# Optimization experiments

Hardware: AMD Instinct MI355X
Metric: run time of the kernel (lower is better)

Reference implementation:

```python
import jax, jax.numpy as jnp
import numpy as np

MAT_MODE = ((0, 1), (0, 2), (1, 2))
VEC_MODE = (2, 1, 0)
DENSITY_SHIFT = -10.0
DISTANCE_SCALE = 25.0


def grid_sample_2d(img, coords):
    # img: [C, H, W]; coords: [N, 2] in [-1, 1], (x indexes W, y indexes H);
    # bilinear, align_corners=True (matches F.grid_sample in the source).
    C, H, W = img.shape
    x = (coords[:, 0] + 1.0) * 0.5 * (W - 1)
    y = (coords[:, 1] + 1.0) * 0.5 * (H - 1)
    x0 = jnp.floor(x)
    y0 = jnp.floor(y)
    wx = x - x0
    wy = y - y0
    x0i = jnp.clip(x0.astype(jnp.int32), 0, W - 1)
    x1i = jnp.clip(x0i + 1, 0, W - 1)
    y0i = jnp.clip(y0.astype(jnp.int32), 0, H - 1)
    y1i = jnp.clip(y0i + 1, 0, H - 1)
    v00 = img[:, y0i, x0i]
    v01 = img[:, y0i, x1i]
    v10 = img[:, y1i, x0i]
    v11 = img[:, y1i, x1i]
    return (v00 * (1 - wx) * (1 - wy) + v01 * wx * (1 - wy)
            + v10 * (1 - wx) * wy + v11 * wx * wy)  # [C, N]


def line_sample_1d(line, t):
    # line: [C, L]; t: [N] in [-1, 1]. Equivalent to the source's grid_sample on a
    # [1, C, L, 1] tensor with coords (0, t): the width dim (size 1) collapses.
    C, L = line.shape
    y = (t + 1.0) * 0.5 * (L - 1)
    y0 = jnp.floor(y)
    wy = y - y0
    y0i = jnp.clip(y0.astype(jnp.int32), 0, L - 1)
    y1i = jnp.clip(y0i + 1, 0, L - 1)
    return line[:, y0i] * (1 - wy) + line[:, y1i] * wy  # [C, N]


def tensorf_features(planes, lines, xyz):
    # planes: [3, C, H, W]; lines: [3, C, L]; xyz: [N, 3] normalized coords.
    # fusion_two='concat' then fusion_one='multiply' == per-plane multiply, concat.
    feats = []
    for i in range(3):
        a, b = MAT_MODE[i]
        pc = jnp.stack([xyz[:, a], xyz[:, b]], axis=-1)  # [N, 2]
        pf = grid_sample_2d(planes[i], pc)               # [C, N]
        lf = line_sample_1d(lines[i], xyz[:, VEC_MODE[i]])  # [C, N]
        feats.append(pf * lf)
    return jnp.concatenate(feats, axis=0)  # [3C, N]


def raw2alpha(sigma, dist):
    # sigma, dist: [Nr, Ns]
    alpha = 1.0 - jnp.exp(-sigma * dist)
    T = jnp.cumprod(jnp.concatenate(
        [jnp.ones((alpha.shape[0], 1), alpha.dtype), 1.0 - alpha + 1e-10], axis=-1), axis=-1)
    weights = alpha * T[:, :-1]
    return alpha, weights, T[:, -1:]


def setup_inputs() -> dict:
    key = jax.random.key(0)
    ks = jax.random.split(key, 10)
    Nr, Ns, G = 4096, 256, 300
    aabb = jnp.array([[-1.5, -1.5, -1.5], [1.5, 1.5, 1.5]], jnp.float32)
    xyz_sampled = jax.random.uniform(ks[0], (Nr, Ns, 3), jnp.float32,
                                     minval=-1.5, maxval=1.5)
    vd = jax.random.normal(ks[1], (Nr, 3), jnp.float32)
    viewdirs = vd / jnp.linalg.norm(vd, axis=-1, keepdims=True)
    near, far = 2.0, 6.0
    t = jnp.linspace(0.0, 1.0, Ns, dtype=jnp.float32)
    z_vals = near * (1.0 - t) + far * t
    z_vals = jnp.broadcast_to(z_vals, (Nr, Ns)) + \
        jax.random.uniform(ks[2], (Nr, Ns), jnp.float32) * ((far - near) / Ns)
    z_vals = jnp.sort(z_vals, axis=-1)
    s = 0.1  # init_scale
    return {
        'xyz_sampled': xyz_sampled,
        'viewdirs': viewdirs,
        'z_vals': z_vals,
        'density_planes': s * jax.random.normal(ks[3], (3, 8, G, G), jnp.float32),
        'density_lines': s * jax.random.normal(ks[4], (3, 8, G), jnp.float32),
        'app_planes': s * jax.random.normal(ks[5], (3, 24, G, G), jnp.float32),
        'app_lines': s * jax.random.normal(ks[6], (3, 24, G), jnp.float32),
        'density_basis_w': jnp.ones((1, 24), jnp.float32),  # source inits to 1/density_dim
        'app_basis_w': s * jax.random.normal(ks[7], (3, 72), jnp.float32),
        'aabb': aabb,
    }


def reference(xyz_sampled, viewdirs, z_vals, density_planes, density_lines,
              app_planes, app_lines, density_basis_w, app_basis_w, aabb):
    Nr, Ns, _ = xyz_sampled.shape
    # normalize_coord: map aabb -> [-1, 1]
    inv_size = 2.0 / (aabb[1] - aabb[0])
    xyz = ((xyz_sampled - aabb[0]) * inv_size - 1.0).reshape(-1, 3)  # [N, 3]

    dfeat = tensorf_features(density_planes, density_lines, xyz)      # [24, N]
    sigma_feat = (density_basis_w @ dfeat).reshape(Nr, Ns)            # basis_mat
    sigma = jax.nn.softplus(sigma_feat + DENSITY_SHIFT)               # fea2denseAct

    # ray-marching distances
    dists = z_vals[:, 1:] - z_vals[:, :-1]
    dists = jnp.concatenate([dists, dists[:, -1:]], axis=-1)
    alpha, weights, bg_T = raw2alpha(sigma, dists * DISTANCE_SCALE)

    # appearance branch: RGBRender is identity on the 3-dim basis output
    afeat = tensorf_features(app_planes, app_lines, xyz)              # [72, N]
    rgb = (app_basis_w @ afeat).T.reshape(Nr, Ns, 3)

    rgb_map = jnp.sum(weights[..., None] * rgb, axis=1)               # [Nr, 3]
    return rgb_map
```

## Files before the change

### kernel.cpp

```cpp
#include <hip/hip_runtime.h>
#include <math.h>

#define G  300
#define NS 256
#define NR 4096
#define CT 32

typedef _Float16 half16_t;
typedef _Float16 h8 __attribute__((ext_vector_type(8)));

__global__ __launch_bounds__(256) void prep_all(
    const float* __restrict__ dp, const float* __restrict__ ap,
    const float* __restrict__ dl, const float* __restrict__ al,
    half16_t* __restrict__ outp, half16_t* __restrict__ outl)
{
  int t = blockIdx.x * blockDim.x + threadIdx.x;
  if (t < 3 * G * G) {
    int x  = t % G;
    int yi = t / G;
    int y  = yi % G;
    int i  = yi / G;
    const float* dpp = dp + ((size_t)(i * 8) * G + y) * G + x;
    const float* app = ap + ((size_t)(i * 24) * G + y) * G + x;
    h8 v[4];
#pragma unroll
    for (int c = 0; c < 8; ++c) v[c >> 3][c & 7] = (half16_t)dpp[(size_t)c * G * G];
#pragma unroll
    for (int c = 0; c < 24; ++c) {
      int cc = c + 8;
      v[cc >> 3][cc & 7] = (half16_t)app[(size_t)c * G * G];
    }
    h8* o = (h8*)(outp + (size_t)t * CT);
#pragma unroll
    for (int m = 0; m < 4; ++m) o[m] = v[m];
  } else {
    int u = t - 3 * G * G;
    if (u < 3 * G) {
      int p = u % G;
      int i = u / G;
      h8 v[4];
#pragma unroll
      for (int c = 0; c < 8; ++c) v[c >> 3][c & 7] = (half16_t)dl[(i * 8 + c) * G + p];
#pragma unroll
      for (int c = 0; c < 24; ++c) {
        int cc = c + 8;
        v[cc >> 3][cc & 7] = (half16_t)al[(i * 24 + c) * G + p];
      }
      h8* o = (h8*)(outl + (size_t)u * CT);
#pragma unroll
      for (int m = 0; m < 4; ++m) o[m] = v[m];
    }
  }
}

__global__ __launch_bounds__(256) void tensorf_fused(
    const float* __restrict__ xyz, const float* __restrict__ zv,
    const half16_t* __restrict__ planes, const half16_t* __restrict__ lns,
    const float* __restrict__ dbw, const float* __restrict__ abw,
    const float* __restrict__ aabb, float* __restrict__ out)
{
  __shared__ float4 srgb[2][NS];
  __shared__ float  sW[3][128];
  __shared__ float  sTot[2];
  __shared__ float4 sSum[2][2];

  const int tid = threadIdx.x;
  for (int idx = tid; idx < 3 * 128; idx += 256) {
    int j = idx >> 7, c = idx & 127;
    float v = 0.f;
    if (c < 72) v = abw[j * 72 + c];
    else if (j == 0 && c < 96) v = dbw[c - 72];
    sW[j][c] = v;
  }
  __syncthreads();

  const int wv   = tid >> 6;
  const int lane = tid & 63;
  const int rl   = wv >> 1;
  const int hf   = wv & 1;
  const int ray  = (blockIdx.x << 1) + rl;
  const int q    = lane >> 2;
  const int r    = lane & 3;

  const float a0x = aabb[0], a0y = aabb[1], a0z = aabb[2];
  const float ivx = 2.f / (aabb[3] - aabb[0]);
  const float ivy = 2.f / (aabb[4] - aabb[1]);
  const float ivz = 2.f / (aabb[5] - aabb[2]);

  const int MA[3] = {0, 0, 1};
  const int MB[3] = {1, 2, 2};
  const int MV[3] = {2, 1, 0};

  const int ro = r * 8;

  for (int it = 0; it < 8; ++it) {
    int s = (hf << 7) + (it << 4) + q;
    const float* xp = xyz + ((size_t)ray * NS + s) * 3;
    float g[3];
    g[0] = (xp[0] - a0x) * ivx - 1.f;
    g[1] = (xp[1] - a0y) * ivy - 1.f;
    g[2] = (xp[2] - a0z) * ivz - 1.f;

    float acc0 = 0.f, acc1 = 0.f, acc2 = 0.f;
#pragma unroll
    for (int i = 0; i < 3; ++i) {
      float fx = (g[MA[i]] + 1.f) * (0.5f * (G - 1));
      float fy = (g[MB[i]] + 1.f) * (0.5f * (G - 1));
      float ft = (g[MV[i]] + 1.f) * (0.5f * (G - 1));
      float x0f = floorf(fx), y0f = floorf(fy), t0f = floorf(ft);
      float wx = fx - x0f, wy = fy - y0f, wt = ft - t0f;
      int x0 = min(max((int)x0f, 0), G - 1);
      int y0 = min(max((int)y0f, 0), G - 1);
      int t0 = min(max((int)t0f, 0), G - 1);
      int x1 = min(x0 + 1, G - 1);
      int y1 = min(y0 + 1, G - 1);
      int t1 = min(t0 + 1, G - 1);

      const half16_t* pb = planes + (size_t)i * G * G * CT;
      h8 t00 = *(const h8*)(pb + ((size_t)(y0 * G + x0)) * CT + ro);
      h8 t01 = *(const h8*)(pb + ((size_t)(y0 * G + x1)) * CT + ro);
      h8 t10 = *(const h8*)(pb + ((size_t)(y1 * G + x0)) * CT + ro);
      h8 t11 = *(const h8*)(pb + ((size_t)(y1 * G + x1)) * CT + ro);
      const half16_t* lb = lns + (size_t)i * G * CT + ro;
      h8 l0 = *(const h8*)(lb + (size_t)t0 * CT);
      h8 l1 = *(const h8*)(lb + (size_t)t1 * CT);

      float w00 = (1.f - wx) * (1.f - wy), w01 = wx * (1.f - wy);
      float w10 = (1.f - wx) * wy,         w11 = wx * wy;
      float wl0 = 1.f - wt;

      float f[8];
#pragma unroll
      for (int k = 0; k < 8; ++k) {
        float pf = (float)t00[k] * w00 + (float)t01[k] * w01
                 + (float)t10[k] * w10 + (float)t11[k] * w11;
        float lf = (float)l0[k] * wl0 + (float)l1[k] * wt;
        f[k] = pf * lf;
      }

      int cb = (r == 0) ? (72 + i * 8) : (i * 24 + (r - 1) * 8);
      const float4* wp0 = (const float4*)&sW[0][cb];
      const float4* wp1 = (const float4*)&sW[1][cb];
      const float4* wp2 = (const float4*)&sW[2][cb];
      float4 wa, wb;
      wa = wp0[0]; wb = wp0[1];
      acc0 += wa.x * f[0] + wa.y * f[1] + wa.z * f[2] + wa.w * f[3]
            + wb.x * f[4] + wb.y * f[5] + wb.z * f[6] + wb.w * f[7];
      wa = wp1[0]; wb = wp1[1];
      acc1 += wa.x * f[0] + wa.y * f[1] + wa.z * f[2] + wa.w * f[3]
            + wb.x * f[4] + wb.y * f[5] + wb.z * f[6] + wb.w * f[7];
      wa = wp2[0]; wb = wp2[1];
      acc2 += wa.x * f[0] + wa.y * f[1] + wa.z * f[2] + wa.w * f[3]
            + wb.x * f[4] + wb.y * f[5] + wb.z * f[6] + wb.w * f[7];
    }
    float4 v;
    v.x = (r == 0) ? acc0 : 0.f;
    v.y = (r == 0) ? 0.f : acc0;
    v.z = (r == 0) ? 0.f : acc1;
    v.w = (r == 0) ? 0.f : acc2;
#pragma unroll
    for (int m = 1; m <= 2; m <<= 1) {
      v.x += __shfl_xor(v.x, m);
      v.y += __shfl_xor(v.y, m);
      v.z += __shfl_xor(v.z, m);
      v.w += __shfl_xor(v.w, m);
    }
    if (r == 0) srgb[rl][s] = v;
  }
  __syncthreads();

  const int s0 = (hf << 7) + (lane << 1);
  const float* zp = zv + (size_t)ray * NS + s0;
  float2 z2 = *(const float2*)zp;
  float d0 = z2.y - z2.x;
  float d1 = (s0 + 2 < NS) ? (zp[2] - z2.y) : d0;

  float4 c0 = srgb[rl][s0];
  float4 c1 = srgb[rl][s0 + 1];

  float vs0 = c0.x - 10.0f;
  float sp0 = (vs0 > 0.f) ? (vs0 + log1pf(expf(-vs0))) : log1pf(expf(vs0));
  float al0 = 1.f - expf(-sp0 * (d0 * 25.0f));
  float vs1 = c1.x - 10.0f;
  float sp1 = (vs1 > 0.f) ? (vs1 + log1pf(expf(-vs1))) : log1pf(expf(vs1));
  float al1 = 1.f - expf(-sp1 * (d1 * 25.0f));

  float tl = (1.f - al0 + 1e-10f) * (1.f - al1 + 1e-10f);

  float incl = tl;
#pragma unroll
  for (int off = 1; off < 64; off <<= 1) {
    float p = __shfl_up(incl, off);
    if (lane >= off) incl *= p;
  }
  float Twave = __shfl_up(incl, 1);
  if (lane == 0) Twave = 1.f;

  if (hf == 0 && lane == 63) sTot[rl] = incl;
  __syncthreads();

  float Tstart = hf ? sTot[rl] : 1.f;
  float T = Tstart * Twave;

  float w0 = al0 * T;
  T *= (1.f - al0 + 1e-10f);
  float w1 = al1 * T;

  float ar = w0 * c0.y + w1 * c1.y;
  float ag = w0 * c0.z + w1 * c1.z;
  float ab = w0 * c0.w + w1 * c1.w;
#pragma unroll
  for (int off = 32; off > 0; off >>= 1) {
    ar += __shfl_down(ar, off);
    ag += __shfl_down(ag, off);
    ab += __shfl_down(ab, off);
  }
  if (lane == 0) sSum[rl][hf] = make_float4(ar, ag, ab, 0.f);
  __syncthreads();

  if (hf == 0 && lane == 0) {
    float4 A = sSum[rl][0];
    float4 B = sSum[rl][1];
    out[ray * 3 + 0] = A.x + B.x;
    out[ray * 3 + 1] = A.y + B.y;
    out[ray * 3 + 2] = A.z + B.z;
  }
}

extern "C" void kernel_launch(void* const* d_in, const int* in_sizes, int n_in,
                              void* d_out, int out_size, void* d_ws, size_t ws_size,
                              hipStream_t stream)
{
  const float* xyz  = (const float*)d_in[0];
  const float* zv   = (const float*)d_in[2];
  const float* dp   = (const float*)d_in[3];
  const float* dl   = (const float*)d_in[4];
  const float* ap   = (const float*)d_in[5];
  const float* al   = (const float*)d_in[6];
  const float* dbw  = (const float*)d_in[7];
  const float* abw  = (const float*)d_in[8];
  const float* aabb = (const float*)d_in[9];
  float* out = (float*)d_out;

  half16_t* planes16 = (half16_t*)d_ws;
  half16_t* lines16  = planes16 + (size_t)3 * G * G * CT;

  hipLaunchKernelGGL(prep_all, dim3((3 * G * G + 3 * G + 255) / 256), dim3(256), 0, stream,
                     dp, ap, dl, al, planes16, lines16);
  hipLaunchKernelGGL(tensorf_fused, dim3(NR / 2), dim3(256), 0, stream,
                     xyz, zv, planes16, lines16, dbw, abw, aabb, out);
}
```

Before: 236.3 us.

## Bin samples into plane row slabs and process plane-by-plane for gather locality

Precomputes per-sample grid coordinates into shared memory, then loops over the three planes and over row slabs of each plane, processing only samples that fall in the current slab and accumulating results into shared memory. This aims to make the texture-like gathers more cache local across the block. It adds extra loop passes with divergent skips, shared-memory read-modify-write accumulation and larger shared memory usage, which can reduce occupancy.

```diff
diff --git a/kernel.cpp b/kernel.cpp
--- a/kernel.cpp
+++ b/kernel.cpp
@@ -5,6 +5,7 @@
 #define NS 256
 #define NR 4096
 #define CT 32
+#define SLABS 4
 
 typedef _Float16 half16_t;
 typedef _Float16 h8 __attribute__((ext_vector_type(8)));
@@ -60,6 +61,8 @@
     const float* __restrict__ aabb, float* __restrict__ out)
 {
   __shared__ float4 srgb[2][NS];
+  __shared__ float2 sFxy[2][3][NS];
+  __shared__ float  sFt [2][3][NS];
   __shared__ float  sW[3][128];
   __shared__ float  sTot[2];
   __shared__ float4 sSum[2][2];
@@ -72,7 +75,6 @@
     else if (j == 0 && c < 96) v = dbw[c - 72];
     sW[j][c] = v;
   }
-  __syncthreads();
 
   const int wv   = tid >> 6;
   const int lane = tid & 63;
@@ -93,79 +95,108 @@
 
   const int ro = r * 8;
 
-  for (int it = 0; it < 8; ++it) {
-    int s = (hf << 7) + (it << 4) + q;
-    const float* xp = xyz + ((size_t)ray * NS + s) * 3;
-    float g[3];
-    g[0] = (xp[0] - a0x) * ivx - 1.f;
-    g[1] = (xp[1] - a0y) * ivy - 1.f;
-    g[2] = (xp[2] - a0z) * ivz - 1.f;
-
-    float acc0 = 0.f, acc1 = 0.f, acc2 = 0.f;
-#pragma unroll
-    for (int i = 0; i < 3; ++i) {
-      float fx = (g[MA[i]] + 1.f) * (0.5f * (G - 1));
-      float fy = (g[MB[i]] + 1.f) * (0.5f * (G - 1));
-      float ft = (g[MV[i]] + 1.f) * (0.5f * (G - 1));
-      float x0f = floorf(fx), y0f = floorf(fy), t0f = floorf(ft);
-      float wx = fx - x0f, wy = fy - y0f, wt = ft - t0f;
-      int x0 = min(max((int)x0f, 0), G - 1);
-      int y0 = min(max((int)y0f, 0), G - 1);
-      int t0 = min(max((int)t0f, 0), G - 1);
-      int x1 = min(x0 + 1, G - 1);
-      int y1 = min(y0 + 1, G - 1);
-      int t1 = min(t0 + 1, G - 1);
-
-      const half16_t* pb = planes + (size_t)i * G * G * CT;
-      h8 t00 = *(const h8*)(pb + ((size_t)(y0 * G + x0)) * CT + ro);
-      h8 t01 = *(const h8*)(pb + ((size_t)(y0 * G + x1)) * CT + ro);
-      h8 t10 = *(const h8*)(pb + ((size_t)(y1 * G + x0)) * CT + ro);
-      h8 t11 = *(const h8*)(pb + ((size_t)(y1 * G + x1)) * CT + ro);
-      const half16_t* lb = lns + (size_t)i * G * CT + ro;
-      h8 l0 = *(const h8*)(lb + (size_t)t0 * CT);
-      h8 l1 = *(const h8*)(lb + (size_t)t1 * CT);
-
-      float w00 = (1.f - wx) * (1.f - wy), w01 = wx * (1.f - wy);
-      float w10 = (1.f - wx) * wy,         w11 = wx * wy;
-      float wl0 = 1.f - wt;
-
-      float f[8];
-#pragma unroll
-      for (int k = 0; k < 8; ++k) {
-        float pf = (float)t00[k] * w00 + (float)t01[k] * w01
-                 + (float)t10[k] * w10 + (float)t11[k] * w11;
-        float lf = (float)l0[k] * wl0 + (float)l1[k] * wt;
-        f[k] = pf * lf;
+  {
+    int sbase = (hf << 7) + (lane << 1);
+#pragma unroll
+    for (int u = 0; u < 2; ++u) {
+      int s = sbase + u;
+      const float* xp = xyz + ((size_t)ray * NS + s) * 3;
+      float g0 = (xp[0] - a0x) * ivx - 1.f;
+      float g1 = (xp[1] - a0y) * ivy - 1.f;
+      float g2 = (xp[2] - a0z) * ivz - 1.f;
+      float g[3] = {g0, g1, g2};
+#pragma unroll
+      for (int i = 0; i < 3; ++i) {
+        float fx = (g[MA[i]] + 1.f) * (0.5f * (G - 1));
+        float fy = (g[MB[i]] + 1.f) * (0.5f * (G - 1));
+        float ft = (g[MV[i]] + 1.f) * (0.5f * (G - 1));
+        sFxy[rl][i][s] = make_float2(fx, fy);
+        sFt [rl][i][s] = ft;
       }
-
-      int cb = (r == 0) ? (72 + i * 8) : (i * 24 + (r - 1) * 8);
-      const float4* wp0 = (const float4*)&sW[0][cb];
-      const float4* wp1 = (const float4*)&sW[1][cb];
-      const float4* wp2 = (const float4*)&sW[2][cb];
-      float4 wa, wb;
-      wa = wp0[0]; wb = wp0[1];
-      acc0 += wa.x * f[0] + wa.y * f[1] + wa.z * f[2] + wa.w * f[3]
-            + wb.x * f[4] + wb.y * f[5] + wb.z * f[6] + wb.w * f[7];
-      wa = wp1[0]; wb = wp1[1];
-      acc1 += wa.x * f[0] + wa.y * f[1] + wa.z * f[2] + wa.w * f[3]
-            + wb.x * f[4] + wb.y * f[5] + wb.z * f[6] + wb.w * f[7];
-      wa = wp2[0]; wb = wp2[1];
-      acc2 += wa.x * f[0] + wa.y * f[1] + wa.z * f[2] + wa.w * f[3]
-            + wb.x * f[4] + wb.y * f[5] + wb.z * f[6] + wb.w * f[7];
-    }
-    float4 v;
-    v.x = (r == 0) ? acc0 : 0.f;
-    v.y = (r == 0) ? 0.f : acc0;
-    v.z = (r == 0) ? 0.f : acc1;
-    v.w = (r == 0) ? 0.f : acc2;
-#pragma unroll
-    for (int m = 1; m <= 2; m <<= 1) {
-      v.x += __shfl_xor(v.x, m);
-      v.y += __shfl_xor(v.y, m);
-      v.z += __shfl_xor(v.z, m);
-      v.w += __shfl_xor(v.w, m);
-    }
-    if (r == 0) srgb[rl][s] = v;
+      srgb[rl][s] = make_float4(0.f, 0.f, 0.f, 0.f);
+    }
+  }
+  __syncthreads();
+
+  const float slabInv = (float)SLABS / (float)G;
+
+  for (int p = 0; p < 3; ++p) {
+    const half16_t* pb = planes + (size_t)p * G * G * CT;
+    const half16_t* lb = lns + (size_t)p * G * CT + ro;
+    const int cb = (r == 0) ? (72 + p * 8) : (p * 24 + (r - 1) * 8);
+
+    for (int sl = 0; sl < SLABS; ++sl) {
+      for (int it = 0; it < 8; ++it) {
+        int s = (hf << 7) + (it << 4) + q;
+        float2 fxy = sFxy[rl][p][s];
+        int slab = (int)(fxy.y * slabInv);
+        if (slab != sl) continue;
+
+        float ft  = sFt[rl][p][s];
+        float x0f = floorf(fxy.x), y0f = floorf(fxy.y), t0f = floorf(ft);
+        float wx = fxy.x - x0f, wy = fxy.y - y0f, wt = ft - t0f;
+        int x0 = min(max((int)x0f, 0), G - 1);
+        int y0 = min(max((int)y0f, 0), G - 1);
+        int t0 = min(max((int)t0f, 0), G - 1);
+        int x1 = min(x0 + 1, G - 1);
+        int y1 = min(y0 + 1, G - 1);
+        int t1 = min(t0 + 1, G - 1);
+
+        h8 t00 = *(const h8*)(pb + ((size_t)(y0 * G + x0)) * CT + ro);
+        h8 t01 = *(const h8*)(pb + ((size_t)(y0 * G + x1)) * CT + ro);
+        h8 t10 = *(const h8*)(pb + ((size_t)(y1 * G + x0)) * CT + ro);
+        h8 t11 = *(const h8*)(pb + ((size_t)(y1 * G + x1)) * CT + ro);
+        h8 l0  = *(const h8*)(lb + (size_t)t0 * CT);
+        h8 l1  = *(const h8*)(lb + (size_t)t1 * CT);
+
+        float w00 = (1.f - wx) * (1.f - wy), w01 = wx * (1.f - wy);
+        float w10 = (1.f - wx) * wy,         w11 = wx * wy;
+        float wl0 = 1.f - wt;
+
+        float acc0 = 0.f, acc1 = 0.f, acc2 = 0.f;
+        {
+          const float4* wp0 = (const float4*)&sW[0][cb];
+          const float4* wp1 = (const float4*)&sW[1][cb];
+          const float4* wp2 = (const float4*)&sW[2][cb];
+          float f[8];
+#pragma unroll
+          for (int k = 0; k < 8; ++k) {
+            float pf = (float)t00[k] * w00 + (float)t01[k] * w01
+                     + (float)t10[k] * w10 + (float)t11[k] * w11;
+            float lf = (float)l0[k] * wl0 + (float)l1[k] * wt;
+            f[k] = pf * lf;
+          }
+          float4 wa, wb;
+          wa = wp0[0]; wb = wp0[1];
+          acc0 = wa.x * f[0] + wa.y * f[1] + wa.z * f[2] + wa.w * f[3]
+               + wb.x * f[4] + wb.y * f[5] + wb.z * f[6] + wb.w * f[7];
+          wa = wp1[0]; wb = wp1[1];
+          acc1 = wa.x * f[0] + wa.y * f[1] + wa.z * f[2] + wa.w * f[3]
+               + wb.x * f[4] + wb.y * f[5] + wb.z * f[6] + wb.w * f[7];
+          wa = wp2[0]; wb = wp2[1];
+          acc2 = wa.x * f[0] + wa.y * f[1] + wa.z * f[2] + wa.w * f[3]
+               + wb.x * f[4] + wb.y * f[5] + wb.z * f[6] + wb.w * f[7];
+        }
+
+        float4 v;
+        v.x = (r == 0) ? acc0 : 0.f;
+        v.y = (r == 0) ? 0.f : acc0;
+        v.z = (r == 0) ? 0.f : acc1;
+        v.w = (r == 0) ? 0.f : acc2;
+#pragma unroll
+        for (int m = 1; m <= 2; m <<= 1) {
+          v.x += __shfl_xor(v.x, m);
+          v.y += __shfl_xor(v.y, m);
+          v.z += __shfl_xor(v.z, m);
+          v.w += __shfl_xor(v.w, m);
+        }
+        if (r == 0) {
+          float4 a = srgb[rl][s];
+          a.x += v.x; a.y += v.y; a.z += v.z; a.w += v.w;
+          srgb[rl][s] = a;
+        }
+      }
+    }
   }
   __syncthreads();
 
@@ -190,8 +221,8 @@
   float incl = tl;
 #pragma unroll
   for (int off = 1; off < 64; off <<= 1) {
-    float p = __shfl_up(incl, off);
-    if (lane >= off) incl *= p;
+    float pp = __shfl_up(incl, off);
+    if (lane >= off) incl *= pp;
   }
   float Twave = __shfl_up(incl, 1);
   if (lane == 0) Twave = 1.f;
```

Measured after the change: 375.6 us. 59.0% more time.

## Reorder ray samples by spatial slab bins to improve gather cache locality

Applied to the files above, without the earlier changes.

Each wave bins its 128 samples into a 6x6 grid of slabs on the y/z coordinates, using ballot and popcount to build a sorted sample index list in shared memory. The gather loop then processes samples in that order, so that lanes processed together touch nearby plane texels and get better L1/L2 reuse. The per-plane loop is also kept rolled to reduce register pressure. In exchange the kernel does an extra pass over xyz, runs a 36-bucket ballot loop, and adds an indirection through shared memory.

```diff
diff --git a/kernel.cpp b/kernel.cpp
--- a/kernel.cpp
+++ b/kernel.cpp
@@ -5,6 +5,7 @@
 #define NS 256
 #define NR 4096
 #define CT 32
+#define SLABS 6
 
 typedef _Float16 half16_t;
 typedef _Float16 h8 __attribute__((ext_vector_type(8)));
@@ -60,8 +61,9 @@
     const float* __restrict__ aabb, float* __restrict__ out)
 {
   __shared__ float4 srgb[2][NS];
-  __shared__ float  sW[3][128];
-  __shared__ float  sTot[2];
+  __shared__ unsigned char lst[4][128];
+  __shared__ float sW[3][128];
+  __shared__ float sTot[2];
   __shared__ float4 sSum[2][2];
 
   const int tid = threadIdx.x;
@@ -72,7 +74,6 @@
     else if (j == 0 && c < 96) v = dbw[c - 72];
     sW[j][c] = v;
   }
-  __syncthreads();
 
   const int wv   = tid >> 6;
   const int lane = tid & 63;
@@ -87,26 +88,58 @@
   const float ivy = 2.f / (aabb[4] - aabb[1]);
   const float ivz = 2.f / (aabb[5] - aabb[2]);
 
-  const int MA[3] = {0, 0, 1};
-  const int MB[3] = {1, 2, 2};
-  const int MV[3] = {2, 1, 0};
+  int key[2];
+  {
+    const float slabScale = (float)SLABS / (float)G;
+#pragma unroll
+    for (int j = 0; j < 2; ++j) {
+      int s = (hf << 7) + (lane << 1) + j;
+      const float* xp = xyz + ((size_t)ray * NS + s) * 3;
+      float g1 = (xp[1] - a0y) * ivy - 1.f;
+      float g2 = (xp[2] - a0z) * ivz - 1.f;
+      float fy0 = (g1 + 1.f) * (0.5f * (G - 1));
+      float fy1 = (g2 + 1.f) * (0.5f * (G - 1));
+      int k0 = min(max((int)(fy0 * slabScale), 0), SLABS - 1);
+      int k1 = min(max((int)(fy1 * slabScale), 0), SLABS - 1);
+      key[j] = k0 * SLABS + k1;
+    }
+  }
+
+  {
+    const unsigned long long ltmask = (1ull << lane) - 1ull;
+    int off = 0;
+    for (int b = 0; b < SLABS * SLABS; ++b) {
+#pragma unroll
+      for (int j = 0; j < 2; ++j) {
+        bool hit = (key[j] == b);
+        unsigned long long m = __ballot(hit);
+        if (hit) lst[wv][off + (int)__popcll(m & ltmask)] =
+                   (unsigned char)((hf << 7) + (lane << 1) + j);
+        off += (int)__popcll(m);
+      }
+    }
+  }
+  __syncthreads();
 
   const int ro = r * 8;
 
-  for (int it = 0; it < 8; ++it) {
-    int s = (hf << 7) + (it << 4) + q;
-    const float* xp = xyz + ((size_t)ray * NS + s) * 3;
-    float g[3];
-    g[0] = (xp[0] - a0x) * ivx - 1.f;
-    g[1] = (xp[1] - a0y) * ivy - 1.f;
-    g[2] = (xp[2] - a0z) * ivz - 1.f;
+  for (int base = 0; base < 128; base += 16) {
+    const int sid = lst[wv][base + q];
+    const float* xp = xyz + ((size_t)ray * NS + sid) * 3;
+    float g0 = (xp[0] - a0x) * ivx - 1.f;
+    float g1 = (xp[1] - a0y) * ivy - 1.f;
+    float g2 = (xp[2] - a0z) * ivz - 1.f;
 
     float acc0 = 0.f, acc1 = 0.f, acc2 = 0.f;
-#pragma unroll
+#pragma unroll 1
     for (int i = 0; i < 3; ++i) {
-      float fx = (g[MA[i]] + 1.f) * (0.5f * (G - 1));
-      float fy = (g[MB[i]] + 1.f) * (0.5f * (G - 1));
-      float ft = (g[MV[i]] + 1.f) * (0.5f * (G - 1));
+      float ga = (i == 2) ? g1 : g0;
+      float gb = (i == 0) ? g1 : g2;
+      float gv = (i == 0) ? g2 : ((i == 1) ? g1 : g0);
+
+      float fx = (ga + 1.f) * (0.5f * (G - 1));
+      float fy = (gb + 1.f) * (0.5f * (G - 1));
+      float ft = (gv + 1.f) * (0.5f * (G - 1));
       float x0f = floorf(fx), y0f = floorf(fy), t0f = floorf(ft);
       float wx = fx - x0f, wy = fy - y0f, wt = ft - t0f;
       int x0 = min(max((int)x0f, 0), G - 1);
@@ -153,6 +186,7 @@
       acc2 += wa.x * f[0] + wa.y * f[1] + wa.z * f[2] + wa.w * f[3]
             + wb.x * f[4] + wb.y * f[5] + wb.z * f[6] + wb.w * f[7];
     }
+
     float4 v;
     v.x = (r == 0) ? acc0 : 0.f;
     v.y = (r == 0) ? 0.f : acc0;
@@ -165,7 +199,7 @@
       v.z += __shfl_xor(v.z, m);
       v.w += __shfl_xor(v.w, m);
     }
-    if (r == 0) srgb[rl][s] = v;
+    if (r == 0) srgb[rl][sid] = v;
   }
   __syncthreads();
 
@@ -190,8 +224,8 @@
   float incl = tl;
 #pragma unroll
   for (int off = 1; off < 64; off <<= 1) {
-    float p = __shfl_up(incl, off);
-    if (lane >= off) incl *= p;
+    float pp = __shfl_up(incl, off);
+    if (lane >= off) incl *= pp;
   }
   float Twave = __shfl_up(incl, 1);
   if (lane == 0) Twave = 1.f;
@@ -240,7 +274,7 @@
   const float* dbw  = (const float*)d_in[7];
   const float* abw  = (const float*)d_in[8];
   const float* aabb = (const float*)d_in[9];
-  float* out = (float*)d_out;
+  float* outp = (float*)d_out;
 
   half16_t* planes16 = (half16_t*)d_ws;
   half16_t* lines16  = planes16 + (size_t)3 * G * G * CT;
@@ -248,5 +282,5 @@
   hipLaunchKernelGGL(prep_all, dim3((3 * G * G + 3 * G + 255) / 256), dim3(256), 0, stream,
                      dp, ap, dl, al, planes16, lines16);
   hipLaunchKernelGGL(tensorf_fused, dim3(NR / 2), dim3(256), 0, stream,
-                     xyz, zv, planes16, lines16, dbw, abw, aabb, out);
+                     xyz, zv, planes16, lines16, dbw, abw, aabb, outp);
 }
```

After: 227.6 us. 1.04x faster.
